# Optimization experiments

Hardware: AMD Instinct MI355X
Metric: run time of the kernel (lower is better)

## Reference

```python
import jax, jax.numpy as jnp
import numpy as np

N_NODES = 50000
N_EDGES = 800000
IN_CH = 256
HID = 256
OUT_CH = 128


def setup_inputs() -> dict:
    key = jax.random.key(0)
    ks = jax.random.split(key, 12)
    x = jax.random.normal(ks[0], (N_NODES, IN_CH), dtype=jnp.float32)
    adj_rows = jnp.sort(jax.random.randint(ks[1], (N_EDGES,), 0, N_NODES, dtype=jnp.int32))
    adj_cols = jax.random.randint(ks[2], (N_EDGES,), 0, N_NODES, dtype=jnp.int32)
    # normalized adjacency weights (~1/degree scale)
    adj_vals = jax.random.uniform(ks[3], (N_EDGES,), dtype=jnp.float32) / 16.0
    def xavier(k, fan_in, fan_out):
        lim = float(np.sqrt(6.0 / (fan_in + fan_out)))
        return jax.random.uniform(k, (fan_in, fan_out), dtype=jnp.float32, minval=-lim, maxval=lim)
    Wa0 = xavier(ks[4], IN_CH, HID)
    Wa1 = xavier(ks[5], HID, HID)
    Wl0 = xavier(ks[6], IN_CH + HID, HID)
    Wl1 = xavier(ks[7], 2 * HID, OUT_CH)
    return {
        'x': x, 'adj_rows': adj_rows, 'adj_cols': adj_cols, 'adj_vals': adj_vals,
        'Wa0': Wa0, 'ba0': jnp.zeros((HID,), jnp.float32),
        'Wa1': Wa1, 'ba1': jnp.zeros((HID,), jnp.float32),
        'Wl0': Wl0, 'bl0': jnp.zeros((HID,), jnp.float32),
        'Wl1': Wl1, 'bl1': jnp.zeros((OUT_CH,), jnp.float32),
    }


def reference(x, adj_rows, adj_cols, adj_vals, Wa0, ba0, Wa1, ba1, Wl0, bl0, Wl1, bl1):
    n = x.shape[0]

    def spmm(h):
        # sparse adj @ h : gather neighbor rows, scale by edge weight, segment-sum into dst
        return jax.ops.segment_sum(adj_vals[:, None] * h[adj_cols], adj_rows, num_segments=n)

    # layer 0
    agg = jax.nn.relu(spmm(x) @ Wa0 + ba0)
    h = jax.nn.relu(jnp.concatenate((x, agg), axis=1) @ Wl0 + bl0)
    # layer 1 (last: no activation after linear)
    agg = jax.nn.relu(spmm(h) @ Wa1 + ba1)
    h = jnp.concatenate((h, agg), axis=1) @ Wl1 + bl1
    # F.normalize: row-wise L2 with eps=1e-12
    norm = jnp.maximum(jnp.linalg.norm(h, axis=1, keepdims=True), 1e-12)
    return h / norm
```

## Files before the change

kernel.cpp:

```cpp
#include <hip/hip_runtime.h>

typedef unsigned short u16;
typedef __attribute__((ext_vector_type(8))) __bf16 bf16x8;
typedef __attribute__((ext_vector_type(4))) float f32x4;
typedef __attribute__((ext_vector_type(8))) u16 u16x8;
typedef __attribute__((ext_vector_type(4))) u16 u16x4;

__device__ __forceinline__ float bf2f(u16 u) {
  return __builtin_bit_cast(float, ((unsigned)u) << 16);
}
__device__ __forceinline__ u16 f2bf(float f) {
  unsigned x = __builtin_bit_cast(unsigned, f);
  x += 0x7fffu + ((x >> 16) & 1u);
  return (u16)(x >> 16);
}
__device__ __forceinline__ f32x4 cvt4(u16x4 v) {
  return (f32x4){bf2f(v.x), bf2f(v.y), bf2f(v.z), bf2f(v.w)};
}
__device__ __forceinline__ void gload_lds16(const void* g, void* l) {
  __builtin_amdgcn_global_load_lds(
      (const __attribute__((address_space(1))) void*)g,
      (__attribute__((address_space(3))) void*)l, 16, 0, 0);
}

__global__ void prepw4_kernel(const float* __restrict__ W0, u16* __restrict__ T0,
                              const float* __restrict__ W1, u16* __restrict__ T1,
                              const float* __restrict__ W2, u16* __restrict__ T2,
                              const float* __restrict__ W3, u16* __restrict__ T3) {
  int i = blockIdx.x * 256 + threadIdx.x;
  const float* W; u16* T; int K, N;
  if (i < 65536)        { W = W0; T = T0; K = 256; N = 256; }
  else if (i < 131072)  { W = W1; T = T1; K = 256; N = 256; i -= 65536; }
  else if (i < 262144)  { W = W2; T = T2; K = 512; N = 256; i -= 131072; }
  else if (i < 327680)  { W = W3; T = T3; K = 512; N = 128; i -= 262144; }
  else return;
  int k = i / N, n = i - k * N;
  T[(size_t)n * K + k] = f2bf(W[i]);
}

__global__ void cvtx_kernel(const float* __restrict__ in, u16* __restrict__ out,
                            int total4) {
  int i = blockIdx.x * 256 + threadIdx.x;
  if (i >= total4) return;
  const float4 v = ((const float4*)in)[i];
  u16x4 o = { f2bf(v.x), f2bf(v.y), f2bf(v.z), f2bf(v.w) };
  ((u16x4*)out)[i] = o;
}

__global__ void rowptr_kernel(const int* __restrict__ rows, int nE,
                              int* __restrict__ rp, int nN) {
  int i = blockIdx.x * 256 + threadIdx.x;
  if (i > nN) return;
  int lo = 0, hi = nE;
  while (lo < hi) { int mid = (lo + hi) >> 1; if (rows[mid] < i) lo = mid + 1; else hi = mid; }
  rp[i] = lo;
}

__global__ __launch_bounds__(128) void spmm_kernel(
    const u16* __restrict__ X, const int* __restrict__ rp,
    const int* __restrict__ cols, const float* __restrict__ vals,
    u16* __restrict__ out, int nN) {
  int lane = threadIdx.x & 63;
  int node = blockIdx.x * 2 + (threadIdx.x >> 6);
  if (node >= nN) return;
  int e0 = rp[node], e1 = rp[node + 1];
  f32x4 s0 = {0.f, 0.f, 0.f, 0.f}, s1 = s0, s2 = s0, s3 = s0;
  const u16* xp = X + (size_t)lane * 4;
  int e = e0;
  for (; e + 4 <= e1; e += 4) {
    int c0 = cols[e], c1 = cols[e + 1], c2 = cols[e + 2], c3 = cols[e + 3];
    float v0 = vals[e], v1 = vals[e + 1], v2 = vals[e + 2], v3 = vals[e + 3];
    u16x4 x0 = *(const u16x4*)(xp + (size_t)c0 * 256);
    u16x4 x1 = *(const u16x4*)(xp + (size_t)c1 * 256);
    u16x4 x2 = *(const u16x4*)(xp + (size_t)c2 * 256);
    u16x4 x3 = *(const u16x4*)(xp + (size_t)c3 * 256);
    s0 += v0 * cvt4(x0);
    s1 += v1 * cvt4(x1);
    s2 += v2 * cvt4(x2);
    s3 += v3 * cvt4(x3);
  }
  for (; e < e1; ++e) {
    int c = cols[e];
    float v = vals[e];
    u16x4 xv = *(const u16x4*)(xp + (size_t)c * 256);
    s0 += v * cvt4(xv);
  }
  f32x4 s = (s0 + s1) + (s2 + s3);
  u16x4 o = { f2bf(s.x), f2bf(s.y), f2bf(s.z), f2bf(s.w) };
  *(u16x4*)(out + (size_t)node * 256 + lane * 4) = o;
}

template<int KTOT, bool SPLIT, bool RELU, bool OUTF32, bool NORM>
__global__ __launch_bounds__(256) void gemm_kernel(
    const u16* __restrict__ A0, const u16* __restrict__ A1,
    const u16* __restrict__ Wt, const float* __restrict__ bias,
    void* __restrict__ outp, int M, int N) {
  __shared__ u16 As[2][128 * 64];
  __shared__ u16 Bs[2][128 * 64];
  __shared__ float red[128][2];

  const int lane = threadIdx.x & 63;
  const int wid = threadIdx.x >> 6;
  const int wr = wid >> 1, wc = wid & 1;
  const int row0b = blockIdx.y * 128;
  const int col0b = blockIdx.x * 128;
  const int lr = lane & 15;
  const int kg = lane >> 4;

  const int u = (wid * 4) * 64 + lane;

  auto stage = [&](int buf, int kt) {
    const u16* Asrc = (!SPLIT || kt < 4) ? A0 : A1;
    const int kkl = (!SPLIT || kt < 4) ? kt * 64 : (kt - 4) * 64;
    #pragma unroll
    for (int i = 0; i < 4; ++i) {
      const int c = wid * 4 + i;
      const int uu = u + i * 64;
      const int row = uu >> 3;
      const int ksd = uu & 7;
      const int kss = ksd ^ (row & 7);
      int grow = row0b + row;
      if (grow >= M) grow = M - 1;
      gload_lds16(Asrc + (size_t)grow * 256 + kkl + kss * 8, &As[buf][c * 512]);
      gload_lds16(Wt + (size_t)(col0b + row) * KTOT + kt * 64 + kss * 8, &Bs[buf][c * 512]);
    }
  };

  f32x4 acc[4][4];
  #pragma unroll
  for (int ni = 0; ni < 4; ++ni) {
    float bv = bias[col0b + wc * 64 + ni * 16 + lr];
    #pragma unroll
    for (int mi = 0; mi < 4; ++mi) acc[mi][ni] = (f32x4){bv, bv, bv, bv};
  }

  constexpr int KSTEPS = KTOT / 64;
  stage(0, 0);
  __syncthreads();

  for (int kt = 0; kt < KSTEPS; ++kt) {
    const int cur = kt & 1;
    if (kt + 1 < KSTEPS) stage(cur ^ 1, kt + 1);

    #pragma unroll
    for (int ks = 0; ks < 2; ++ks) {
      const int q = ks * 4 + kg;
      bf16x8 a[4], b[4];
      #pragma unroll
      for (int mi = 0; mi < 4; ++mi) {
        const int r = wr * 64 + mi * 16 + lr;
        a[mi] = __builtin_bit_cast(bf16x8,
            *(const u16x8*)&As[cur][r * 64 + (q ^ (r & 7)) * 8]);
      }
      #pragma unroll
      for (int ni = 0; ni < 4; ++ni) {
        const int cb = wc * 64 + ni * 16 + lr;
        b[ni] = __builtin_bit_cast(bf16x8,
            *(const u16x8*)&Bs[cur][cb * 64 + (q ^ (cb & 7)) * 8]);
      }
      #pragma unroll
      for (int mi = 0; mi < 4; ++mi)
        #pragma unroll
        for (int ni = 0; ni < 4; ++ni)
          acc[mi][ni] = __builtin_amdgcn_mfma_f32_16x16x32_bf16(a[mi], b[ni], acc[mi][ni], 0, 0, 0);
    }
    __syncthreads();
  }

  float invn[4][4];
  if (NORM) {
    #pragma unroll
    for (int mi = 0; mi < 4; ++mi) {
      #pragma unroll
      for (int j = 0; j < 4; ++j) {
        float p = 0.f;
        #pragma unroll
        for (int ni = 0; ni < 4; ++ni) { float v = acc[mi][ni][j]; p += v * v; }
        #pragma unroll
        for (int m = 1; m < 16; m <<= 1) p += __shfl_xor(p, m, 64);
        int rl = wr * 64 + mi * 16 + kg * 4 + j;
        if (lr == 0) red[rl][wc] = p;
        invn[mi][j] = 0.f;
      }
    }
    __syncthreads();
    #pragma unroll
    for (int mi = 0; mi < 4; ++mi) {
      #pragma unroll
      for (int j = 0; j < 4; ++j) {
        int rl = wr * 64 + mi * 16 + kg * 4 + j;
        float ss = red[rl][0] + red[rl][1];
        float nrm = sqrtf(ss);
        nrm = nrm > 1e-12f ? nrm : 1e-12f;
        invn[mi][j] = 1.f / nrm;
      }
    }
  }

  #pragma unroll
  for (int mi = 0; mi < 4; ++mi) {
    #pragma unroll
    for (int j = 0; j < 4; ++j) {
      int r = row0b + wr * 64 + mi * 16 + kg * 4 + j;
      if (r >= M) continue;
      #pragma unroll
      for (int ni = 0; ni < 4; ++ni) {
        float v = acc[mi][ni][j];
        if (RELU) v = v > 0.f ? v : 0.f;
        if (NORM) v *= invn[mi][j];
        int c = col0b + wc * 64 + ni * 16 + lr;
        if (OUTF32) ((float*)outp)[(size_t)r * N + c] = v;
        else        ((u16*)outp)[(size_t)r * N + c] = f2bf(v);
      }
    }
  }
}

extern "C" void kernel_launch(void* const* d_in, const int* in_sizes, int n_in,
                              void* d_out, int out_size, void* d_ws, size_t ws_size,
                              hipStream_t stream) {
  const float* x        = (const float*)d_in[0];
  const int*   adj_rows = (const int*)d_in[1];
  const int*   adj_cols = (const int*)d_in[2];
  const float* adj_vals = (const float*)d_in[3];
  const float* Wa0 = (const float*)d_in[4];
  const float* ba0 = (const float*)d_in[5];
  const float* Wa1 = (const float*)d_in[6];
  const float* ba1 = (const float*)d_in[7];
  const float* Wl0 = (const float*)d_in[8];
  const float* bl0 = (const float*)d_in[9];
  const float* Wl1 = (const float*)d_in[10];
  const float* bl1 = (const float*)d_in[11];

  const int nN = in_sizes[0] / 256;
  const int nE = in_sizes[1];

  char* ws = (char*)d_ws;
  size_t off = 0;
  auto alloc = [&](size_t bytes) -> void* {
    void* p = ws + off;
    off += (bytes + 255) & ~(size_t)255;
    return p;
  };
  u16* x_bf  = (u16*)alloc((size_t)nN * 256 * 2);
  u16* aggA  = (u16*)alloc((size_t)nN * 256 * 2);
  u16* aggB  = (u16*)alloc((size_t)nN * 256 * 2);
  u16* h_bf  = (u16*)alloc((size_t)nN * 256 * 2);
  int* rp    = (int*)alloc((size_t)(nN + 1) * 4);
  u16* wt_a0 = (u16*)alloc(256 * 256 * 2);
  u16* wt_a1 = (u16*)alloc(256 * 256 * 2);
  u16* wt_l0 = (u16*)alloc(512 * 256 * 2);
  u16* wt_l1 = (u16*)alloc(512 * 128 * 2);
  if (off > ws_size) return;

  dim3 blk(256);
  prepw4_kernel<<<dim3(1280), blk, 0, stream>>>(Wa0, wt_a0, Wa1, wt_a1, Wl0, wt_l0, Wl1, wt_l1);
  cvtx_kernel<<<dim3((nN * 64 + 255) / 256), blk, 0, stream>>>(x, x_bf, nN * 64);
  rowptr_kernel<<<dim3((nN + 1 + 255) / 256), blk, 0, stream>>>(adj_rows, nE, rp, nN);

  const int MB = (nN + 127) / 128;
  dim3 gN256(2, MB);
  dim3 gN128(1, MB);
  dim3 gNode((nN + 1) / 2);
  dim3 sblk(128);

  spmm_kernel<<<gNode, sblk, 0, stream>>>(x_bf, rp, adj_cols, adj_vals, aggA, nN);
  gemm_kernel<256, false, true, false, false><<<gN256, blk, 0, stream>>>(aggA, nullptr, wt_a0, ba0, aggB, nN, 256);
  gemm_kernel<512, true, true, false, false><<<gN256, blk, 0, stream>>>(x_bf, aggB, wt_l0, bl0, h_bf, nN, 256);
  spmm_kernel<<<gNode, sblk, 0, stream>>>(h_bf, rp, adj_cols, adj_vals, aggA, nN);
  gemm_kernel<256, false, true, false, false><<<gN256, blk, 0, stream>>>(aggA, nullptr, wt_a1, ba1, aggB, nN, 256);
  gemm_kernel<512, true, false, true, true><<<gN128, blk, 0, stream>>>(h_bf, aggB, wt_l1, bl1, (float*)d_out, nN, 128);
}
```

Before: 227.3 us.

## Tile SpMM gather over column ranges to improve cache locality

The SpMM kernel now walks each node's edge list eight times, and on each pass it only gathers neighbours whose column index falls in one eighth of the node range. The aim is that concurrently running waves touch a smaller working set of feature rows at a time, which should improve L2/MALL hit rates. In exchange, the column and index reads are repeated eight times per node and the per-edge branches cause divergence. There is also no cross-wave synchronisation, so waves can drift out of step with each other's tiles.

Result: slower. 452.4 us (+99.1%).

```diff
diff --git a/kernel.cpp b/kernel.cpp
--- a/kernel.cpp
+++ b/kernel.cpp
@@ -59,31 +59,44 @@
 __global__ __launch_bounds__(128) void spmm_kernel(
     const u16* __restrict__ X, const int* __restrict__ rp,
     const int* __restrict__ cols, const float* __restrict__ vals,
-    u16* __restrict__ out, int nN) {
+    u16* __restrict__ out, int nN, int tileSz) {
   int lane = threadIdx.x & 63;
   int node = blockIdx.x * 2 + (threadIdx.x >> 6);
   if (node >= nN) return;
   int e0 = rp[node], e1 = rp[node + 1];
   f32x4 s0 = {0.f, 0.f, 0.f, 0.f}, s1 = s0, s2 = s0, s3 = s0;
   const u16* xp = X + (size_t)lane * 4;
-  int e = e0;
-  for (; e + 4 <= e1; e += 4) {
-    int c0 = cols[e], c1 = cols[e + 1], c2 = cols[e + 2], c3 = cols[e + 3];
-    float v0 = vals[e], v1 = vals[e + 1], v2 = vals[e + 2], v3 = vals[e + 3];
-    u16x4 x0 = *(const u16x4*)(xp + (size_t)c0 * 256);
-    u16x4 x1 = *(const u16x4*)(xp + (size_t)c1 * 256);
-    u16x4 x2 = *(const u16x4*)(xp + (size_t)c2 * 256);
-    u16x4 x3 = *(const u16x4*)(xp + (size_t)c3 * 256);
-    s0 += v0 * cvt4(x0);
-    s1 += v1 * cvt4(x1);
-    s2 += v2 * cvt4(x2);
-    s3 += v3 * cvt4(x3);
-  }
-  for (; e < e1; ++e) {
-    int c = cols[e];
-    float v = vals[e];
-    u16x4 xv = *(const u16x4*)(xp + (size_t)c * 256);
-    s0 += v * cvt4(xv);
+
+  for (int t = 0; t < 8; ++t) {
+    const int clo = t * tileSz;
+    const int chi = clo + tileSz;
+    int e = e0;
+    for (; e + 4 <= e1; e += 4) {
+      int c0 = cols[e], c1 = cols[e + 1], c2 = cols[e + 2], c3 = cols[e + 3];
+      if (c0 >= clo && c0 < chi) {
+        float v = vals[e];
+        s0 += v * cvt4(*(const u16x4*)(xp + (size_t)c0 * 256));
+      }
+      if (c1 >= clo && c1 < chi) {
+        float v = vals[e + 1];
+        s1 += v * cvt4(*(const u16x4*)(xp + (size_t)c1 * 256));
+      }
+      if (c2 >= clo && c2 < chi) {
+        float v = vals[e + 2];
+        s2 += v * cvt4(*(const u16x4*)(xp + (size_t)c2 * 256));
+      }
+      if (c3 >= clo && c3 < chi) {
+        float v = vals[e + 3];
+        s3 += v * cvt4(*(const u16x4*)(xp + (size_t)c3 * 256));
+      }
+    }
+    for (; e < e1; ++e) {
+      int c = cols[e];
+      if (c >= clo && c < chi) {
+        float v = vals[e];
+        s0 += v * cvt4(*(const u16x4*)(xp + (size_t)c * 256));
+      }
+    }
   }
   f32x4 s = (s0 + s1) + (s2 + s3);
   u16x4 o = { f2bf(s.x), f2bf(s.y), f2bf(s.z), f2bf(s.w) };
@@ -234,6 +247,7 @@
 
   const int nN = in_sizes[0] / 256;
   const int nE = in_sizes[1];
+  const int tileSz = (nN + 7) / 8;
 
   char* ws = (char*)d_ws;
   size_t off = 0;
@@ -264,10 +278,10 @@
   dim3 gNode((nN + 1) / 2);
   dim3 sblk(128);
 
-  spmm_kernel<<<gNode, sblk, 0, stream>>>(x_bf, rp, adj_cols, adj_vals, aggA, nN);
+  spmm_kernel<<<gNode, sblk, 0, stream>>>(x_bf, rp, adj_cols, adj_vals, aggA, nN, tileSz);
   gemm_kernel<256, false, true, false, false><<<gN256, blk, 0, stream>>>(aggA, nullptr, wt_a0, ba0, aggB, nN, 256);
   gemm_kernel<512, true, true, false, false><<<gN256, blk, 0, stream>>>(x_bf, aggB, wt_l0, bl0, h_bf, nN, 256);
-  spmm_kernel<<<gNode, sblk, 0, stream>>>(h_bf, rp, adj_cols, adj_vals, aggA, nN);
+  spmm_kernel<<<gNode, sblk, 0, stream>>>(h_bf, rp, adj_cols, adj_vals, aggA, nN, tileSz);
   gemm_kernel<256, false, true, false, false><<<gN256, blk, 0, stream>>>(aggA, nullptr, wt_a1, ba1, aggB, nN, 256);
   gemm_kernel<512, true, false, true, true><<<gN128, blk, 0, stream>>>(h_bf, aggB, wt_l1, bl1, (float*)d_out, nN, 128);
 }
```
